# Kernel tuning notes

Measured on AMD Instinct MI355X. Metric: run time of the kernel, lower is better.

The kernel has to match this reference:

```python
import jax, jax.numpy as jnp
import numpy as np

L_LAYERS = 6  # weight-tied layer count
ROPE_BASE = 10000.0
LN_EPS = 1e-5


def _ln(x):
    # LayerNorm over last dim, no affine (elementwise_affine=False)
    m = x.mean(-1, keepdims=True)
    v = ((x - m) ** 2).mean(-1, keepdims=True)
    return (x - m) * jax.lax.rsqrt(v + LN_EPS)


def _rope(x):
    # x: (B,H,T,d), d even. Pairs are adjacent (even,odd) indices, cos/sin
    # repeat_interleave(2) pattern, matching the torch implementation.
    d, T = x.shape[-1], x.shape[-2]
    inv_freq = 1.0 / (ROPE_BASE ** (jnp.arange(0, d, 2, dtype=x.dtype) / d))  # (d/2,)
    freqs = jnp.arange(T, dtype=x.dtype)[:, None] * inv_freq[None, :]  # (T, d/2)
    cos, sin = jnp.cos(freqs), jnp.sin(freqs)
    xe, xo = x[..., ::2], x[..., 1::2]
    oe = xe * cos - xo * sin
    oo = xo * cos + xe * sin
    return jnp.stack([oe, oo], axis=-1).reshape(x.shape)


def _attn(Q, K, V):
    # Q,K: (B,H,T,d_head); V: (B,T,D). RoPE + causal softmax, heads averaged.
    d = Q.shape[-1]
    T = Q.shape[-2]
    Qr, Kr = _rope(Q), _rope(K)
    scale = 1.0 / jnp.sqrt(jnp.asarray(d, Q.dtype))
    scores = jnp.einsum('bhtd,bhsd->bhts', Qr, Kr) * scale  # (B,H,T,T)
    causal = jnp.tril(jnp.ones((T, T), dtype=bool))
    scores = jnp.where(causal, scores, -jnp.inf)
    attn = jax.nn.softmax(scores, axis=-1)
    # mean over heads of (attn @ V) == (mean over heads of attn) @ V since V is shared
    attn_mean = attn.mean(axis=1)  # (B,T,T)
    return jnp.einsum('bts,bsd->btd', attn_mean, V)  # (B,T,D)


def setup_inputs() -> dict:
    key = jax.random.key(0)
    ks = jax.random.split(key, 6)
    B, T, D, H, N, V = 2, 256, 256, 4, 32768, 32000
    n = N // H
    std = 0.02
    return {
        'idx': jax.random.randint(ks[0], (B, T), 0, V, dtype=jnp.int32),
        'wte': jax.random.normal(ks[1], (V, D), jnp.float32) * std,
        'encoder': jax.random.normal(ks[2], (N, D), jnp.float32) * std,
        'decoder_x': jax.random.normal(ks[3], (H, D, n), jnp.float32) * std,
        'decoder_y': jax.random.normal(ks[4], (H, D, n), jnp.float32) * std,
        'readout': jax.random.normal(ks[5], (D, V), jnp.float32) * std,
    }


def reference(idx, wte, encoder, decoder_x, decoder_y, readout):
    B, T = idx.shape
    H, D, n = decoder_x.shape
    N = H * n
    v = _ln(wte[idx])  # (B,T,D)
    for _ in range(L_LAYERS):  # weight-tied repeats
        x = jax.nn.relu(jnp.einsum('btd,hdn->bhtn', v, decoder_x))  # (B,H,T,n)
        a = _attn(x, x, v)  # (B,T,D)
        y = jax.nn.relu(jnp.einsum('btd,hdn->bhtn', _ln(a), decoder_y)) * x
        y_flat = y.transpose(0, 2, 1, 3).reshape(B, T, N)  # head-major concat
        v = _ln(v + _ln(y_flat @ encoder))
    return v @ readout  # logits (B,T,vocab)
```

## Files before the change

kernel.cpp:

```cpp
#include <hip/hip_runtime.h>
#include <hip/hip_bf16.h>
#include <math.h>

#define BB   2
#define TT   256
#define DD   256
#define HH   4
#define NN   32768
#define nn   8192
#define VV   32000
#define L_LAYERS 6
#define LN_EPS 1e-5f

typedef __attribute__((ext_vector_type(8))) short bf16x8;
typedef __attribute__((ext_vector_type(4))) float f32x4;

__device__ __forceinline__ unsigned short f2bf(float f) {
    union { float f; unsigned int u; } v; v.f = f;
    unsigned int r = (v.u + 0x7FFFu + ((v.u >> 16) & 1u)) >> 16;
    return (unsigned short)r;
}
__device__ __forceinline__ float bf2f(unsigned short h) {
    union { unsigned int u; float f; } v; v.u = ((unsigned int)h) << 16;
    return v.f;
}
__device__ __forceinline__ bf16x8 ld_frag(const unsigned short* p) {
    union { bf16x8 v; uint2 u[2]; } r;
    r.u[0] = *(const uint2*)(p);
    r.u[1] = *(const uint2*)(p + 4);
    return r.v;
}

__device__ __forceinline__ float block_sum(float v) {
    __shared__ float sh[4];
    #pragma unroll
    for (int o = 32; o > 0; o >>= 1) v += __shfl_down(v, o, 64);
    __syncthreads();
    if ((threadIdx.x & 63) == 0) sh[threadIdx.x >> 6] = v;
    __syncthreads();
    return sh[0] + sh[1] + sh[2] + sh[3];
}
__device__ __forceinline__ float block_max(float v) {
    __shared__ float sh[4];
    #pragma unroll
    for (int o = 32; o > 0; o >>= 1) v = fmaxf(v, __shfl_down(v, o, 64));
    __syncthreads();
    if ((threadIdx.x & 63) == 0) sh[threadIdx.x >> 6] = v;
    __syncthreads();
    return fmaxf(fmaxf(sh[0], sh[1]), fmaxf(sh[2], sh[3]));
}
__device__ __forceinline__ float ln_val(float x) {
    float m = block_sum(x) * (1.0f / 256.0f);
    float d = x - m;
    float var = block_sum(d * d) * (1.0f / 256.0f);
    return d * rsqrtf(var + LN_EPS);
}

__global__ __launch_bounds__(256) void embed_ln_k(const int* __restrict__ idx,
                                                  const float* __restrict__ wte,
                                                  float* __restrict__ v,
                                                  unsigned short* __restrict__ vb) {
    int row = blockIdx.x;
    int tok = idx[row];
    float x = wte[(size_t)tok * DD + threadIdx.x];
    float o = ln_val(x);
    size_t i = (size_t)row * DD + threadIdx.x;
    v[i] = o;
    vb[i] = f2bf(o);
}

__global__ __launch_bounds__(256) void ln_rows_k(const float* __restrict__ in,
                                                 unsigned short* __restrict__ ob) {
    size_t i = (size_t)blockIdx.x * DD + threadIdx.x;
    ob[i] = f2bf(ln_val(in[i]));
}

__global__ __launch_bounds__(256) void add_ln_ln_k(float* __restrict__ v,
                                                   const float* __restrict__ yenc,
                                                   unsigned short* __restrict__ vb) {
    size_t i = (size_t)blockIdx.x * DD + threadIdx.x;
    float t1 = ln_val(yenc[i]);
    float w = v[i] + t1;
    float o = ln_val(w);
    v[i] = o;
    vb[i] = f2bf(o);
}

__global__ __launch_bounds__(256) void tconv_k(const float* __restrict__ src,
                                               unsigned short* __restrict__ dst,
                                               int R, int C, long sstride, long dstride) {
    src += (size_t)blockIdx.z * sstride;
    dst += (size_t)blockIdx.z * dstride;
    __shared__ unsigned short tile[64][66];
    int c0 = blockIdx.x * 64, r0 = blockIdx.y * 64;
    int c = threadIdx.x & 63, q = threadIdx.x >> 6;
    #pragma unroll
    for (int i = 0; i < 16; i++) {
        int r = q + i * 4;
        tile[r][c] = f2bf(src[(size_t)(r0 + r) * C + c0 + c]);
    }
    __syncthreads();
    #pragma unroll
    for (int i = 0; i < 16; i++) {
        int r = q + i * 4;
        dst[(size_t)(c0 + r) * R + r0 + c] = tile[c][r];
    }
}

__device__ __forceinline__ void bt_mainloop(const unsigned short* Ap, long lda,
                                            const unsigned short* Bp, long ldb,
                                            int ksteps,
                                            unsigned short (*As)[36],
                                            unsigned short (*Bs)[36],
                                            f32x4 (&acc)[4][4]) {
    int tid = threadIdx.x;
    int ra = tid >> 1, pa = (tid & 1) * 16;
    int lane = tid & 63, w = tid >> 6;
    int rowoff = (w >> 1) * 64, coloff = (w & 1) * 64;
    int fr = lane & 15, fq = (lane >> 4) * 8;
    const unsigned short* ga = Ap + (size_t)ra * lda + pa;
    const unsigned short* gb = Bp + (size_t)ra * ldb + pa;
    uint4 a0 = *(const uint4*)ga, a1 = *(const uint4*)(ga + 8);
    uint4 b0 = *(const uint4*)gb, b1 = *(const uint4*)(gb + 8);
    for (int k = 0; k < ksteps; k++) {
        __syncthreads();
        uint2* da = (uint2*)&As[ra][pa];
        da[0] = make_uint2(a0.x, a0.y); da[1] = make_uint2(a0.z, a0.w);
        da[2] = make_uint2(a1.x, a1.y); da[3] = make_uint2(a1.z, a1.w);
        uint2* db = (uint2*)&Bs[ra][pa];
        db[0] = make_uint2(b0.x, b0.y); db[1] = make_uint2(b0.z, b0.w);
        db[2] = make_uint2(b1.x, b1.y); db[3] = make_uint2(b1.z, b1.w);
        if (k + 1 < ksteps) {
            ga += 32; gb += 32;
            a0 = *(const uint4*)ga; a1 = *(const uint4*)(ga + 8);
            b0 = *(const uint4*)gb; b1 = *(const uint4*)(gb + 8);
        }
        __syncthreads();
        bf16x8 af[4], bfv[4];
        #pragma unroll
        for (int mi = 0; mi < 4; mi++) af[mi] = ld_frag(&As[rowoff + mi * 16 + fr][fq]);
        #pragma unroll
        for (int nj = 0; nj < 4; nj++) bfv[nj] = ld_frag(&Bs[coloff + nj * 16 + fr][fq]);
        #pragma unroll
        for (int mi = 0; mi < 4; mi++)
            #pragma unroll
            for (int nj = 0; nj < 4; nj++)
                acc[mi][nj] = __builtin_amdgcn_mfma_f32_16x16x32_bf16(af[mi], bfv[nj], acc[mi][nj], 0, 0, 0);
    }
}

__global__ __launch_bounds__(256) void gemm_head_bt(const unsigned short* __restrict__ A,
                                                    const unsigned short* __restrict__ Wt,
                                                    unsigned short* __restrict__ Cx,
                                                    const unsigned short* __restrict__ mulx,
                                                    unsigned short* __restrict__ Cy,
                                                    int mode) {
    int h = blockIdx.z;
    int n0 = blockIdx.x * 128, m0 = blockIdx.y * 128;
    __shared__ __attribute__((aligned(16))) unsigned short smem[16384];
    unsigned short (*As)[36] = (unsigned short (*)[36])smem;
    unsigned short (*Bs)[36] = (unsigned short (*)[36])(smem + 128 * 36);
    f32x4 acc[4][4] = {};
    bt_mainloop(A + (size_t)m0 * DD, DD,
                Wt + (size_t)h * nn * DD + (size_t)n0 * DD, DD, 8, As, Bs, acc);
    __syncthreads();

    int tid = threadIdx.x, lane = tid & 63, w = tid >> 6;
    int rowoff = (w >> 1) * 64, coloff = (w & 1) * 64;
    int r4 = (lane >> 4) * 4, cc = lane & 15;
    unsigned short (*Cs)[128] = (unsigned short (*)[128])smem;
    #pragma unroll
    for (int mi = 0; mi < 4; mi++)
        #pragma unroll
        for (int nj = 0; nj < 4; nj++)
            #pragma unroll
            for (int rr = 0; rr < 4; rr++)
                Cs[rowoff + mi * 16 + r4 + rr][coloff + nj * 16 + cc] =
                    f2bf(fmaxf(acc[mi][nj][rr], 0.0f));
    __syncthreads();

    int colc = (tid & 15) * 8;
    #pragma unroll
    for (int j = 0; j < 8; j++) {
        int row = (tid >> 4) + j * 16;
        int m = m0 + row;
        int b = m >> 8, t = m & 255;
        union { uint4 u; unsigned short s[8]; } ch;
        ch.u = *(const uint4*)&Cs[row][colc];
        if (mode == 0) {
            size_t bhtn = (((size_t)(b * HH + h)) * TT + t) * (size_t)nn + n0 + colc;
            *(uint4*)(Cx + bhtn) = ch.u;
            union { uint4 u; unsigned short s[8]; } ro;
            float tf = (float)t;
            int pbase = ((n0 + colc) >> 1);
            #pragma unroll
            for (int k2 = 0; k2 < 4; k2++) {
                int p = pbase + k2;
                float inv = __expf(-(float)p * (9.210340371976184f / 4096.0f));
                float ang = tf * inv;
                float s = __sinf(ang), c = __cosf(ang);
                float xe = bf2f(ch.s[2 * k2]), xo = bf2f(ch.s[2 * k2 + 1]);
                ro.s[2 * k2]     = f2bf(xe * c - xo * s);
                ro.s[2 * k2 + 1] = f2bf(xo * c + xe * s);
            }
            *(uint4*)(Cy + bhtn) = ro.u;
        } else {
            size_t bhtn = (((size_t)(b * HH + h)) * TT + t) * (size_t)nn + n0 + colc;
            union { uint4 u; unsigned short s[8]; } mx, oy;
            mx.u = *(const uint4*)(mulx + bhtn);
            #pragma unroll
            for (int k2 = 0; k2 < 8; k2++)
                oy.s[k2] = f2bf(bf2f(ch.s[k2]) * bf2f(mx.s[k2]));
            *(uint4*)(Cy + ((size_t)(b * TT + t)) * NN + (size_t)h * nn + n0 + colc) = oy.u;
        }
    }
}

__global__ __launch_bounds__(256) void scores_bt(const unsigned short* __restrict__ xrb,
                                                 float* __restrict__ sc) {
    int zh = blockIdx.z, kc = blockIdx.y, tile = blockIdx.x;
    int t0 = (tile >= 1) ? 128 : 0;
    int s0 = (tile == 2) ? 128 : 0;
    const unsigned short* Xz = xrb + (size_t)zh * TT * nn + (size_t)kc * 512;
    __shared__ unsigned short As[128][36], Bs[128][36];
    f32x4 acc[4][4] = {};
    bt_mainloop(Xz + (size_t)t0 * nn, nn, Xz + (size_t)s0 * nn, nn, 16, As, Bs, acc);
    const float scale = 0.011048543456039805f;
    int tid = threadIdx.x, lane = tid & 63, w = tid >> 6;
    int rowoff = (w >> 1) * 64, coloff = (w & 1) * 64;
    int r4 = (lane >> 4) * 4, cc = lane & 15;
    float* scz = sc + (size_t)zh * TT * TT;
    #pragma unroll
    for (int mi = 0; mi < 4; mi++)
        #pragma unroll
        for (int nj = 0; nj < 4; nj++)
            #pragma unroll
            for (int rr = 0; rr < 4; rr++) {
                int t = t0 + rowoff + mi * 16 + r4 + rr;
                int s = s0 + coloff + nj * 16 + cc;
                atomicAdd(&scz[(size_t)t * TT + s], acc[mi][nj][rr] * scale);
            }
}

__global__ __launch_bounds__(256) void gemm_enc_bt(const unsigned short* __restrict__ A,
                                                   const unsigned short* __restrict__ Bt,
                                                   float* __restrict__ C) {
    int n0 = blockIdx.x * 128, m0 = blockIdx.y * 128;
    long kbase = (long)blockIdx.z * 1024;
    __shared__ unsigned short As[128][36], Bs[128][36];
    f32x4 acc[4][4] = {};
    bt_mainloop(A + (size_t)m0 * NN + kbase, NN,
                Bt + (size_t)n0 * NN + kbase, NN, 32, As, Bs, acc);
    int tid = threadIdx.x, lane = tid & 63, w = tid >> 6;
    int rowoff = (w >> 1) * 64, coloff = (w & 1) * 64;
    int r4 = (lane >> 4) * 4, cc = lane & 15;
    #pragma unroll
    for (int mi = 0; mi < 4; mi++)
        #pragma unroll
        for (int nj = 0; nj < 4; nj++)
            #pragma unroll
            for (int rr = 0; rr < 4; rr++) {
                int row = m0 + rowoff + mi * 16 + r4 + rr;
                int col = n0 + coloff + nj * 16 + cc;
                atomicAdd(&C[(size_t)row * DD + col], acc[mi][nj][rr]);
            }
}

__global__ __launch_bounds__(256) void gemm_ro_bt(const unsigned short* __restrict__ A,
                                                  const unsigned short* __restrict__ Wt,
                                                  float* __restrict__ out) {
    int n0 = blockIdx.x * 128, m0 = blockIdx.y * 128;
    __shared__ unsigned short As[128][36], Bs[128][36];
    f32x4 acc[4][4] = {};
    bt_mainloop(A + (size_t)m0 * DD, DD, Wt + (size_t)n0 * DD, DD, 8, As, Bs, acc);
    int tid = threadIdx.x, lane = tid & 63, w = tid >> 6;
    int rowoff = (w >> 1) * 64, coloff = (w & 1) * 64;
    int r4 = (lane >> 4) * 4, cc = lane & 15;
    #pragma unroll
    for (int mi = 0; mi < 4; mi++)
        #pragma unroll
        for (int nj = 0; nj < 4; nj++)
            #pragma unroll
            for (int rr = 0; rr < 4; rr++) {
                int m = m0 + rowoff + mi * 16 + r4 + rr;
                int col = n0 + coloff + nj * 16 + cc;
                out[(size_t)m * VV + col] = acc[mi][nj][rr];
            }
}

__global__ __launch_bounds__(256) void softmax_mean_k(const float* __restrict__ sc,
                                                      float* __restrict__ am) {
    int bt = blockIdx.x;
    int b = bt >> 8, t = bt & 255;
    int s = threadIdx.x;
    float acc = 0.0f;
    for (int h = 0; h < HH; h++) {
        const float* row = sc + (((size_t)(b * HH + h)) * TT + t) * TT;
        float val = (s <= t) ? row[s] : -1e30f;
        float mx = block_max(val);
        float e = (s <= t) ? expf(val - mx) : 0.0f;
        float sum = block_sum(e);
        acc += e / sum;
    }
    am[((size_t)b * TT + t) * TT + s] = acc * 0.25f;
}

__global__ __launch_bounds__(256) void gemm_nn_k(const float* __restrict__ A,
                                                 const float* __restrict__ B,
                                                 float* __restrict__ C,
                                                 int M, int N, int K,
                                                 long lda, long ldb, long ldc,
                                                 long sAz, long sBz, long sCz) {
    int batch = blockIdx.z;
    A += (size_t)batch * sAz;
    B += (size_t)batch * sBz;
    C += (size_t)batch * sCz;
    int m0 = blockIdx.y * 64, n0 = blockIdx.x * 64;
    __shared__ float As[16][68];
    __shared__ float Bs[16][64];
    int tid = threadIdx.x;
    int tx = tid & 15, ty = tid >> 4;
    int ar = tid >> 2, ac = (tid & 3) * 4;
    int br = tid >> 4, bc = (tid & 15) * 4;
    float acc[4][4] = {};
    for (int k0 = 0; k0 < K; k0 += 16) {
        float4 av = *(const float4*)(A + (size_t)(m0 + ar) * lda + k0 + ac);
        float4 bv = *(const float4*)(B + (size_t)(k0 + br) * ldb + n0 + bc);
        As[ac + 0][ar] = av.x; As[ac + 1][ar] = av.y;
        As[ac + 2][ar] = av.z; As[ac + 3][ar] = av.w;
        *(float4*)&Bs[br][bc] = bv;
        __syncthreads();
        #pragma unroll
        for (int k = 0; k < 16; k++) {
            float4 a4 = *(const float4*)&As[k][ty * 4];
            float4 b4 = *(const float4*)&Bs[k][tx * 4];
            float aa[4] = {a4.x, a4.y, a4.z, a4.w};
            float bb[4] = {b4.x, b4.y, b4.z, b4.w};
            #pragma unroll
            for (int i = 0; i < 4; i++)
                #pragma unroll
                for (int j = 0; j < 4; j++)
                    acc[i][j] = fmaf(aa[i], bb[j], acc[i][j]);
        }
        __syncthreads();
    }
    #pragma unroll
    for (int i = 0; i < 4; i++) {
        int m = m0 + ty * 4 + i;
        #pragma unroll
        for (int j = 0; j < 4; j++) {
            int col = n0 + tx * 4 + j;
            C[(size_t)m * ldc + col] = acc[i][j];
        }
    }
}

extern "C" void kernel_launch(void* const* d_in, const int* in_sizes, int n_in,
                              void* d_out, int out_size, void* d_ws, size_t ws_size,
                              hipStream_t stream) {
    const int*   idx  = (const int*)d_in[0];
    const float* wte  = (const float*)d_in[1];
    const float* enc  = (const float*)d_in[2];
    const float* Wx   = (const float*)d_in[3];
    const float* Wy   = (const float*)d_in[4];
    const float* Wro  = (const float*)d_in[5];
    float* out = (float*)d_out;

    float* ws   = (float*)d_ws;
    float* v    = ws;
    float* sc   = v    + 131072;
    float* am   = sc   + 524288;
    float* a    = am   + 131072;
    float* yenc = a    + 131072;
    unsigned short* sbase = (unsigned short*)(yenc + 131072);
    unsigned short* vb   = sbase;
    unsigned short* lAb  = vb   + 131072;
    unsigned short* xb   = lAb  + 131072;
    unsigned short* xrb  = xb   + 16777216;
    unsigned short* WxT  = xrb  + 16777216;
    unsigned short* WyT  = WxT  + 8388608;
    unsigned short* encT = WyT  + 8388608;
    unsigned short* ybf  = xrb;
    unsigned short* WroT = xb;

    tconv_k<<<dim3(nn / 64, DD / 64, HH), 256, 0, stream>>>(Wx, WxT, DD, nn,
        (long)DD * nn, (long)nn * DD);
    tconv_k<<<dim3(DD / 64, NN / 64, 1), 256, 0, stream>>>(enc, encT, NN, DD, 0L, 0L);
    tconv_k<<<dim3(nn / 64, DD / 64, HH), 256, 0, stream>>>(Wy, WyT, DD, nn,
        (long)DD * nn, (long)nn * DD);

    embed_ln_k<<<BB * TT, 256, 0, stream>>>(idx, wte, v, vb);

    for (int l = 0; l < L_LAYERS; l++) {
        gemm_head_bt<<<dim3(nn / 128, (BB * TT) / 128, HH), 256, 0, stream>>>(
            vb, WxT, xb, nullptr, xrb, 0);

        hipMemsetAsync(sc, 0, (size_t)524288 * sizeof(float), stream);
        scores_bt<<<dim3(3, 16, BB * HH), 256, 0, stream>>>(xrb, sc);

        softmax_mean_k<<<BB * TT, 256, 0, stream>>>(sc, am);

        gemm_nn_k<<<dim3(DD / 64, TT / 64, BB), 256, 0, stream>>>(
            am, v, a, TT, DD, TT,
            (long)TT, (long)DD, (long)DD,
            (long)TT * TT, (long)TT * DD, (long)TT * DD);

        ln_rows_k<<<BB * TT, 256, 0, stream>>>(a, lAb);

        gemm_head_bt<<<dim3(nn / 128, (BB * TT) / 128, HH), 256, 0, stream>>>(
            lAb, WyT, nullptr, xb, ybf, 1);

        hipMemsetAsync(yenc, 0, (size_t)131072 * sizeof(float), stream);
        gemm_enc_bt<<<dim3(2, 4, 32), 256, 0, stream>>>(ybf, encT, yenc);

        add_ln_ln_k<<<BB * TT, 256, 0, stream>>>(v, yenc, vb);
    }

    tconv_k<<<dim3(VV / 64, DD / 64, 1), 256, 0, stream>>>(Wro, WroT, DD, VV, 0L, 0L);

    gemm_ro_bt<<<dim3(VV / 128, (BB * TT) / 128, 1), 256, 0, stream>>>(vb, WroT, out);
}
```

Measured before the change: 1.121 ms.

## Double-buffer GEMM mainloop with direct global-to-LDS loads and finer split-K

```diff
diff --git a/kernel.cpp b/kernel.cpp
--- a/kernel.cpp
+++ b/kernel.cpp
@@ -24,11 +24,15 @@
     union { unsigned int u; float f; } v; v.u = ((unsigned int)h) << 16;
     return v.f;
 }
-__device__ __forceinline__ bf16x8 ld_frag(const unsigned short* p) {
-    union { bf16x8 v; uint2 u[2]; } r;
-    r.u[0] = *(const uint2*)(p);
-    r.u[1] = *(const uint2*)(p + 4);
+__device__ __forceinline__ bf16x8 ld_frag16(const unsigned short* p) {
+    union { bf16x8 v; uint4 u; } r;
+    r.u = *(const uint4*)p;
     return r.v;
+}
+__device__ __forceinline__ void gll16(const unsigned short* g, unsigned short* l) {
+    __builtin_amdgcn_global_load_lds(
+        (const __attribute__((address_space(1))) unsigned int*)g,
+        (__attribute__((address_space(3))) unsigned int*)l, 16, 0, 0);
 }
 
 __device__ __forceinline__ float block_sum(float v) {
@@ -110,42 +114,43 @@
 __device__ __forceinline__ void bt_mainloop(const unsigned short* Ap, long lda,
                                             const unsigned short* Bp, long ldb,
                                             int ksteps,
-                                            unsigned short (*As)[36],
-                                            unsigned short (*Bs)[36],
+                                            unsigned short* As,
+                                            unsigned short* Bs,
                                             f32x4 (&acc)[4][4]) {
-    int tid = threadIdx.x;
-    int ra = tid >> 1, pa = (tid & 1) * 16;
-    int lane = tid & 63, w = tid >> 6;
+    int tid = threadIdx.x, w = tid >> 6, l = tid & 63;
     int rowoff = (w >> 1) * 64, coloff = (w & 1) * 64;
-    int fr = lane & 15, fq = (lane >> 4) * 8;
-    const unsigned short* ga = Ap + (size_t)ra * lda + pa;
-    const unsigned short* gb = Bp + (size_t)ra * ldb + pa;
-    uint4 a0 = *(const uint4*)ga, a1 = *(const uint4*)(ga + 8);
-    uint4 b0 = *(const uint4*)gb, b1 = *(const uint4*)(gb + 8);
+    int fr = l & 15, fq = (l >> 4) * 8;
+    int srow = w * 16 + (l >> 2), scol = (l & 3) * 8;
+    const unsigned short* ga = Ap + (size_t)srow * lda + scol;
+    const unsigned short* gb = Bp + (size_t)srow * ldb + scol;
+    unsigned short* la = As + w * 512;
+    unsigned short* lb = Bs + w * 512;
+    long a64 = 64 * lda, b64 = 64 * ldb;
+    gll16(ga, la);        gll16(ga + a64, la + 2048);
+    gll16(gb, lb);        gll16(gb + b64, lb + 2048);
+    ga += 32; gb += 32;
+    __syncthreads();
     for (int k = 0; k < ksteps; k++) {
-        __syncthreads();
-        uint2* da = (uint2*)&As[ra][pa];
-        da[0] = make_uint2(a0.x, a0.y); da[1] = make_uint2(a0.z, a0.w);
-        da[2] = make_uint2(a1.x, a1.y); da[3] = make_uint2(a1.z, a1.w);
-        uint2* db = (uint2*)&Bs[ra][pa];
-        db[0] = make_uint2(b0.x, b0.y); db[1] = make_uint2(b0.z, b0.w);
-        db[2] = make_uint2(b1.x, b1.y); db[3] = make_uint2(b1.z, b1.w);
+        int cur = (k & 1) * 4096;
+        int nxt = 4096 - cur;
         if (k + 1 < ksteps) {
+            gll16(ga, la + nxt);        gll16(ga + a64, la + nxt + 2048);
+            gll16(gb, lb + nxt);        gll16(gb + b64, lb + nxt + 2048);
             ga += 32; gb += 32;
-            a0 = *(const uint4*)ga; a1 = *(const uint4*)(ga + 8);
-            b0 = *(const uint4*)gb; b1 = *(const uint4*)(gb + 8);
         }
-        __syncthreads();
         bf16x8 af[4], bfv[4];
         #pragma unroll
-        for (int mi = 0; mi < 4; mi++) af[mi] = ld_frag(&As[rowoff + mi * 16 + fr][fq]);
-        #pragma unroll
-        for (int nj = 0; nj < 4; nj++) bfv[nj] = ld_frag(&Bs[coloff + nj * 16 + fr][fq]);
+        for (int mi = 0; mi < 4; mi++)
+            af[mi] = ld_frag16(&As[cur + (rowoff + mi * 16 + fr) * 32 + fq]);
+        #pragma unroll
+        for (int nj = 0; nj < 4; nj++)
+            bfv[nj] = ld_frag16(&Bs[cur + (coloff + nj * 16 + fr) * 32 + fq]);
         #pragma unroll
         for (int mi = 0; mi < 4; mi++)
             #pragma unroll
             for (int nj = 0; nj < 4; nj++)
                 acc[mi][nj] = __builtin_amdgcn_mfma_f32_16x16x32_bf16(af[mi], bfv[nj], acc[mi][nj], 0, 0, 0);
+        __syncthreads();
     }
 }
 
@@ -158,8 +163,8 @@
     int h = blockIdx.z;
     int n0 = blockIdx.x * 128, m0 = blockIdx.y * 128;
     __shared__ __attribute__((aligned(16))) unsigned short smem[16384];
-    unsigned short (*As)[36] = (unsigned short (*)[36])smem;
-    unsigned short (*Bs)[36] = (unsigned short (*)[36])(smem + 128 * 36);
+    unsigned short* As = smem;
+    unsigned short* Bs = smem + 8192;
     f32x4 acc[4][4] = {};
     bt_mainloop(A + (size_t)m0 * DD, DD,
                 Wt + (size_t)h * nn * DD + (size_t)n0 * DD, DD, 8, As, Bs, acc);
@@ -221,10 +226,10 @@
     int zh = blockIdx.z, kc = blockIdx.y, tile = blockIdx.x;
     int t0 = (tile >= 1) ? 128 : 0;
     int s0 = (tile == 2) ? 128 : 0;
-    const unsigned short* Xz = xrb + (size_t)zh * TT * nn + (size_t)kc * 512;
-    __shared__ unsigned short As[128][36], Bs[128][36];
+    const unsigned short* Xz = xrb + (size_t)zh * TT * nn + (size_t)kc * 256;
+    __shared__ __attribute__((aligned(16))) unsigned short As[8192], Bs[8192];
     f32x4 acc[4][4] = {};
-    bt_mainloop(Xz + (size_t)t0 * nn, nn, Xz + (size_t)s0 * nn, nn, 16, As, Bs, acc);
+    bt_mainloop(Xz + (size_t)t0 * nn, nn, Xz + (size_t)s0 * nn, nn, 8, As, Bs, acc);
     const float scale = 0.011048543456039805f;
     int tid = threadIdx.x, lane = tid & 63, w = tid >> 6;
     int rowoff = (w >> 1) * 64, coloff = (w & 1) * 64;
@@ -246,11 +251,11 @@
                                                    const unsigned short* __restrict__ Bt,
                                                    float* __restrict__ C) {
     int n0 = blockIdx.x * 128, m0 = blockIdx.y * 128;
-    long kbase = (long)blockIdx.z * 1024;
-    __shared__ unsigned short As[128][36], Bs[128][36];
+    long kbase = (long)blockIdx.z * 512;
+    __shared__ __attribute__((aligned(16))) unsigned short As[8192], Bs[8192];
     f32x4 acc[4][4] = {};
     bt_mainloop(A + (size_t)m0 * NN + kbase, NN,
-                Bt + (size_t)n0 * NN + kbase, NN, 32, As, Bs, acc);
+                Bt + (size_t)n0 * NN + kbase, NN, 16, As, Bs, acc);
     int tid = threadIdx.x, lane = tid & 63, w = tid >> 6;
     int rowoff = (w >> 1) * 64, coloff = (w & 1) * 64;
     int r4 = (lane >> 4) * 4, cc = lane & 15;
@@ -270,7 +275,7 @@
                                                   const unsigned short* __restrict__ Wt,
                                                   float* __restrict__ out) {
     int n0 = blockIdx.x * 128, m0 = blockIdx.y * 128;
-    __shared__ unsigned short As[128][36], Bs[128][36];
+    __shared__ __attribute__((aligned(16))) unsigned short As[8192], Bs[8192];
     f32x4 acc[4][4] = {};
     bt_mainloop(A + (size_t)m0 * DD, DD, Wt + (size_t)n0 * DD, DD, 8, As, Bs, acc);
     int tid = threadIdx.x, lane = tid & 63, w = tid >> 6;
@@ -369,10 +374,10 @@
     float* ws   = (float*)d_ws;
     float* v    = ws;
     float* sc   = v    + 131072;
-    float* am   = sc   + 524288;
+    float* yenc = sc   + 524288;
+    float* am   = yenc + 131072;
     float* a    = am   + 131072;
-    float* yenc = a    + 131072;
-    unsigned short* sbase = (unsigned short*)(yenc + 131072);
+    unsigned short* sbase = (unsigned short*)(a + 131072);
     unsigned short* vb   = sbase;
     unsigned short* lAb  = vb   + 131072;
     unsigned short* xb   = lAb  + 131072;
@@ -395,8 +400,9 @@
         gemm_head_bt<<<dim3(nn / 128, (BB * TT) / 128, HH), 256, 0, stream>>>(
             vb, WxT, xb, nullptr, xrb, 0);
 
-        hipMemsetAsync(sc, 0, (size_t)524288 * sizeof(float), stream);
-        scores_bt<<<dim3(3, 16, BB * HH), 256, 0, stream>>>(xrb, sc);
+        hipMemsetAsync(sc, 0, (size_t)(524288 + 131072) * sizeof(float), stream);
+
+        scores_bt<<<dim3(3, 32, BB * HH), 256, 0, stream>>>(xrb, sc);
 
         softmax_mean_k<<<BB * TT, 256, 0, stream>>>(sc, am);
 
@@ -410,8 +416,7 @@
         gemm_head_bt<<<dim3(nn / 128, (BB * TT) / 128, HH), 256, 0, stream>>>(
             lAb, WyT, nullptr, xb, ybf, 1);
 
-        hipMemsetAsync(yenc, 0, (size_t)131072 * sizeof(float), stream);
-        gemm_enc_bt<<<dim3(2, 4, 32), 256, 0, stream>>>(ybf, encT, yenc);
+        gemm_enc_bt<<<dim3(2, 4, 64), 256, 0, stream>>>(ybf, encT, yenc);
 
         add_ln_ln_k<<<BB * TT, 256, 0, stream>>>(v, yenc, vb);
     }
```

Result: slower. 1.305 ms (+16.4%).

## Replace atomic split-K accumulation with partial buffers reduced in consumer kernels

Applied to the files above, without the earlier changes.

```diff
diff --git a/kernel.cpp b/kernel.cpp
--- a/kernel.cpp
+++ b/kernel.cpp
@@ -11,6 +11,9 @@
 #define VV   32000
 #define L_LAYERS 6
 #define LN_EPS 1e-5f
+
+#define SKC  4
+#define EKC  16
 
 typedef __attribute__((ext_vector_type(8))) short bf16x8;
 typedef __attribute__((ext_vector_type(4))) float f32x4;
@@ -76,10 +79,14 @@
 }
 
 __global__ __launch_bounds__(256) void add_ln_ln_k(float* __restrict__ v,
-                                                   const float* __restrict__ yenc,
+                                                   const float* __restrict__ yencp,
                                                    unsigned short* __restrict__ vb) {
     size_t i = (size_t)blockIdx.x * DD + threadIdx.x;
-    float t1 = ln_val(yenc[i]);
+    float ysum = 0.0f;
+    #pragma unroll
+    for (int kc = 0; kc < EKC; kc++)
+        ysum += yencp[(size_t)kc * (BB * TT * DD) + i];
+    float t1 = ln_val(ysum);
     float w = v[i] + t1;
     float o = ln_val(w);
     v[i] = o;
@@ -217,43 +224,46 @@
 }
 
 __global__ __launch_bounds__(256) void scores_bt(const unsigned short* __restrict__ xrb,
-                                                 float* __restrict__ sc) {
+                                                 float* __restrict__ scp) {
     int zh = blockIdx.z, kc = blockIdx.y, tile = blockIdx.x;
     int t0 = (tile >= 1) ? 128 : 0;
     int s0 = (tile == 2) ? 128 : 0;
-    const unsigned short* Xz = xrb + (size_t)zh * TT * nn + (size_t)kc * 512;
+    const unsigned short* Xz = xrb + (size_t)zh * TT * nn + (size_t)kc * (nn / SKC);
     __shared__ unsigned short As[128][36], Bs[128][36];
     f32x4 acc[4][4] = {};
-    bt_mainloop(Xz + (size_t)t0 * nn, nn, Xz + (size_t)s0 * nn, nn, 16, As, Bs, acc);
+    bt_mainloop(Xz + (size_t)t0 * nn, nn, Xz + (size_t)s0 * nn, nn, (nn / SKC) / 32,
+                As, Bs, acc);
     const float scale = 0.011048543456039805f;
     int tid = threadIdx.x, lane = tid & 63, w = tid >> 6;
     int rowoff = (w >> 1) * 64, coloff = (w & 1) * 64;
     int r4 = (lane >> 4) * 4, cc = lane & 15;
-    float* scz = sc + (size_t)zh * TT * TT;
+    float* dst = scp + ((size_t)(zh * 3 + tile) * SKC + kc) * 16384;
     #pragma unroll
     for (int mi = 0; mi < 4; mi++)
         #pragma unroll
         for (int nj = 0; nj < 4; nj++)
             #pragma unroll
             for (int rr = 0; rr < 4; rr++) {
-                int t = t0 + rowoff + mi * 16 + r4 + rr;
-                int s = s0 + coloff + nj * 16 + cc;
-                atomicAdd(&scz[(size_t)t * TT + s], acc[mi][nj][rr] * scale);
+                int r = rowoff + mi * 16 + r4 + rr;
+                int c = coloff + nj * 16 + cc;
+                dst[r * 128 + c] = acc[mi][nj][rr] * scale;
             }
 }
 
 __global__ __launch_bounds__(256) void gemm_enc_bt(const unsigned short* __restrict__ A,
                                                    const unsigned short* __restrict__ Bt,
-                                                   float* __restrict__ C) {
+                                                   float* __restrict__ yencp) {
     int n0 = blockIdx.x * 128, m0 = blockIdx.y * 128;
-    long kbase = (long)blockIdx.z * 1024;
+    int kc = blockIdx.z;
+    long kbase = (long)kc * (NN / EKC);
     __shared__ unsigned short As[128][36], Bs[128][36];
     f32x4 acc[4][4] = {};
     bt_mainloop(A + (size_t)m0 * NN + kbase, NN,
-                Bt + (size_t)n0 * NN + kbase, NN, 32, As, Bs, acc);
+                Bt + (size_t)n0 * NN + kbase, NN, (NN / EKC) / 32, As, Bs, acc);
     int tid = threadIdx.x, lane = tid & 63, w = tid >> 6;
     int rowoff = (w >> 1) * 64, coloff = (w & 1) * 64;
     int r4 = (lane >> 4) * 4, cc = lane & 15;
+    float* C = yencp + (size_t)kc * (BB * TT * DD);
     #pragma unroll
     for (int mi = 0; mi < 4; mi++)
         #pragma unroll
@@ -262,7 +272,7 @@
             for (int rr = 0; rr < 4; rr++) {
                 int row = m0 + rowoff + mi * 16 + r4 + rr;
                 int col = n0 + coloff + nj * 16 + cc;
-                atomicAdd(&C[(size_t)row * DD + col], acc[mi][nj][rr]);
+                C[(size_t)row * DD + col] = acc[mi][nj][rr];
             }
 }
 
@@ -288,15 +298,25 @@
             }
 }
 
-__global__ __launch_bounds__(256) void softmax_mean_k(const float* __restrict__ sc,
+__global__ __launch_bounds__(256) void softmax_mean_k(const float* __restrict__ scp,
                                                       float* __restrict__ am) {
     int bt = blockIdx.x;
     int b = bt >> 8, t = bt & 255;
     int s = threadIdx.x;
+    int tr = t & 127, scol = s & 127;
+    int tileid = (t >= 128) ? ((s >= 128) ? 2 : 1) : 0;
     float acc = 0.0f;
     for (int h = 0; h < HH; h++) {
-        const float* row = sc + (((size_t)(b * HH + h)) * TT + t) * TT;
-        float val = (s <= t) ? row[s] : -1e30f;
+        int zh = b * HH + h;
+        float val = -1e30f;
+        if (s <= t) {
+            const float* p = scp + ((size_t)(zh * 3 + tileid) * SKC) * 16384
+                           + tr * 128 + scol;
+            float v0 = 0.0f;
+            #pragma unroll
+            for (int kc = 0; kc < SKC; kc++) v0 += p[(size_t)kc * 16384];
+            val = v0;
+        }
         float mx = block_max(val);
         float e = (s <= t) ? expf(val - mx) : 0.0f;
         float sum = block_sum(e);
@@ -368,11 +388,10 @@
 
     float* ws   = (float*)d_ws;
     float* v    = ws;
-    float* sc   = v    + 131072;
-    float* am   = sc   + 524288;
-    float* a    = am   + 131072;
-    float* yenc = a    + 131072;
-    unsigned short* sbase = (unsigned short*)(yenc + 131072);
+    float* am   = v   + 131072;
+    float* a    = am  + 131072;
+    float* red  = a   + 131072;
+    unsigned short* sbase = (unsigned short*)(red + 2097152);
     unsigned short* vb   = sbase;
     unsigned short* lAb  = vb   + 131072;
     unsigned short* xb   = lAb  + 131072;
@@ -395,10 +414,9 @@
         gemm_head_bt<<<dim3(nn / 128, (BB * TT) / 128, HH), 256, 0, stream>>>(
             vb, WxT, xb, nullptr, xrb, 0);
 
-        hipMemsetAsync(sc, 0, (size_t)524288 * sizeof(float), stream);
-        scores_bt<<<dim3(3, 16, BB * HH), 256, 0, stream>>>(xrb, sc);
-
-        softmax_mean_k<<<BB * TT, 256, 0, stream>>>(sc, am);
+        scores_bt<<<dim3(3, SKC, BB * HH), 256, 0, stream>>>(xrb, red);
+
+        softmax_mean_k<<<BB * TT, 256, 0, stream>>>(red, am);
 
         gemm_nn_k<<<dim3(DD / 64, TT / 64, BB), 256, 0, stream>>>(
             am, v, a, TT, DD, TT,
@@ -410,10 +428,9 @@
         gemm_head_bt<<<dim3(nn / 128, (BB * TT) / 128, HH), 256, 0, stream>>>(
             lAb, WyT, nullptr, xb, ybf, 1);
 
-        hipMemsetAsync(yenc, 0, (size_t)131072 * sizeof(float), stream);
-        gemm_enc_bt<<<dim3(2, 4, 32), 256, 0, stream>>>(ybf, encT, yenc);
-
-        add_ln_ln_k<<<BB * TT, 256, 0, stream>>>(v, yenc, vb);
+        gemm_enc_bt<<<dim3(2, 4, EKC), 256, 0, stream>>>(ybf, encT, red);
+
+        add_ln_ln_k<<<BB * TT, 256, 0, stream>>>(v, red, vb);
     }
 
     tconv_k<<<dim3(VV / 64, DD / 64, 1), 256, 0, stream>>>(Wro, WroT, DD, VV, 0L, 0L);
```

After: 1.172 ms. 4.5% more time.
